# Kernel optimization log

Measured on AMD Instinct MI355X. Metric: run time of the kernel, lower is better.

## Reference

```python
import jax, jax.numpy as jnp
import numpy as np

N = 100_000        # nodes
E_HALF = 1_600_000 # undirected edges; symmetrized -> 3.2M directed
N_IN, N_HEMB, N_HGCN, N_OUT = 128, 32, 32, 1


def setup_inputs() -> dict:
    key = jax.random.key(0)
    ks = jax.random.split(key, 8)
    x = jax.random.normal(ks[0], (N, N_IN), dtype=jnp.float32)
    t = jax.random.uniform(ks[1], (N,), dtype=jnp.float32)
    # symmetric edge list (A = A^T), matching the typical undirected-graph usage
    src = jax.random.randint(ks[2], (E_HALF,), 0, N)
    dst = jax.random.randint(ks[3], (E_HALF,), 0, N)
    row = jnp.concatenate([src, dst]).astype(jnp.int32)
    col = jnp.concatenate([dst, src]).astype(jnp.int32)
    s = 0.05
    W_emb = jax.random.normal(ks[4], (N_IN, N_HEMB), jnp.float32) * s
    b_emb = jnp.zeros((N_HEMB,), jnp.float32)
    W_gcn = jax.random.normal(ks[5], (N_HEMB, N_HGCN), jnp.float32) * s
    b_gcn = jnp.zeros((N_HGCN,), jnp.float32)
    W1 = jax.random.normal(ks[6], (N_HGCN + 2, N_HEMB), jnp.float32) * s
    b1 = jnp.zeros((N_HEMB,), jnp.float32)
    W2 = jax.random.normal(ks[7], (N_HEMB, N_OUT), jnp.float32) * s
    b2 = jnp.zeros((N_OUT,), jnp.float32)
    return dict(x=x, t=t, row=row, col=col,
                W_emb=W_emb, b_emb=b_emb, W_gcn=W_gcn, b_gcn=b_gcn,
                W1=W1, b1=b1, W2=W2, b2=b2)


def reference(x, t, row, col, W_emb, b_emb, W_gcn, b_gcn, W1, b1, W2, b2):
    n = x.shape[0]
    h = jax.nn.relu(x @ W_emb + b_emb)                        # [N, Hemb]
    # per-edge attention score via gather + dot
    att = jnp.einsum('eh,eh->e', h[row], h[col])              # [E]
    att = jnp.exp(att - att.max())                            # global-max stabilized exp
    # per-node softmax denominator (segment sum over neighbors) + eps
    deno = jax.ops.segment_sum(att, row, num_segments=n) + 1e-8
    att = att / deno[row]                                     # normalized edge attention
    # exposure z: attention-weighted neighbor treatments
    z = jax.ops.segment_sum(att * t[col], row, num_segments=n)  # [N]
    # GCNConv (unit edge values: set_value() is non-inplace so adj_t stays valueless;
    # PyG then fills 1s, adds self loops, symmetric D^-1/2 norm)
    deg = jax.ops.segment_sum(jnp.ones(row.shape, jnp.float32), col, num_segments=n) + 1.0
    dis = jax.lax.rsqrt(deg)                                  # [N], deg >= 1
    hw = h @ W_gcn                                            # [N, Hgcn]
    msg = dis[row][:, None] * hw[row]                         # [E, Hgcn]
    agg = jax.ops.segment_sum(msg, col, num_segments=n)       # [N, Hgcn]
    gcn = dis[:, None] * agg + (dis * dis)[:, None] * hw + b_gcn
    rep = h + jax.nn.relu(gcn)                                # residual node rep
    feats = jnp.concatenate([rep, t[:, None], z[:, None]], axis=1)  # [N, Hgcn+2]
    out = jax.nn.relu(feats @ W1 + b1) @ W2 + b2              # [N, 1]
    return out, rep, z
```

## Files before the change

### kernel.cpp

```cpp
#include <hip/hip_runtime.h>
#include <hip/hip_bf16.h>

static constexpr int HN = 32;
static constexpr int NIN = 128;
static constexpr int CH1 = 8192;
static constexpr int CAP2 = 16384;

__device__ __forceinline__ float bf2f(unsigned short u) {
    union { unsigned int i; float f; } v;
    v.i = ((unsigned int)u) << 16;
    return v.f;
}
__device__ __forceinline__ float ldf(const void* p, size_t i, int isbf) {
    return isbf ? bf2f(((const unsigned short*)p)[i]) : ((const float*)p)[i];
}

__global__ void detect_kernel(const unsigned int* __restrict__ xw,
                              int* __restrict__ flag)
{
    int lane = threadIdx.x;
    int hits = 0;
    #pragma unroll
    for (int k = 0; k < 2; ++k) {
        unsigned int w = xw[lane + 64 * k];
        float a = bf2f((unsigned short)(w & 0xFFFFu));
        float aa = fabsf(a);
        if (a == 0.0f || (aa >= 0.000244140625f && aa <= 32.0f)) hits++;
    }
    #pragma unroll
    for (int m = 32; m; m >>= 1) hits += __shfl_xor(hits, m, 64);
    if (lane == 0) flag[0] = (hits >= 64) ? 1 : 0;
}

__global__ __launch_bounds__(256) void embed1_kernel(
    const void* __restrict__ x,
    const void* __restrict__ Wemb,
    const void* __restrict__ bemb,
    const int* __restrict__ flagp,
    float* __restrict__ h, int N)
{
    __shared__ float We[NIN * HN];
    __shared__ float be[HN];
    __shared__ float xs[32][NIN];
    const int tid = threadIdx.x;
    const int isbf = flagp[0];

    for (int i = tid; i < NIN * HN; i += 256) We[i] = ldf(Wemb, i, isbf);
    if (tid < HN) be[tid] = ldf(bemb, tid, isbf);

    const int n0 = blockIdx.x * 32;
    if (isbf) {
        const ushort4* x4 = (const ushort4*)((const unsigned short*)x + (size_t)n0 * NIN);
        for (int i = tid; i < 32 * (NIN / 4); i += 256) {
            ushort4 u = x4[i];
            int base = i * 4, n = base >> 7, k = base & (NIN - 1);
            xs[n][k] = bf2f(u.x); xs[n][k + 1] = bf2f(u.y);
            xs[n][k + 2] = bf2f(u.z); xs[n][k + 3] = bf2f(u.w);
        }
    } else {
        const float4* x4 = (const float4*)((const float*)x + (size_t)n0 * NIN);
        for (int i = tid; i < 32 * (NIN / 4); i += 256) {
            float4 u = x4[i];
            int base = i * 4, n = base >> 7, k = base & (NIN - 1);
            xs[n][k] = u.x; xs[n][k + 1] = u.y;
            xs[n][k + 2] = u.z; xs[n][k + 3] = u.w;
        }
    }
    __syncthreads();

    const int f = tid & 31, ns = tid >> 5;
    float a0 = be[f], a1 = be[f], a2 = be[f], a3 = be[f];
    #pragma unroll 8
    for (int k = 0; k < NIN; ++k) {
        float w = We[k * HN + f];
        a0 += xs[ns +  0][k] * w;
        a1 += xs[ns +  8][k] * w;
        a2 += xs[ns + 16][k] * w;
        a3 += xs[ns + 24][k] * w;
    }
    if (n0 + ns      < N) h[(size_t)(n0 + ns     ) * HN + f] = fmaxf(a0, 0.f);
    if (n0 + ns +  8 < N) h[(size_t)(n0 + ns +  8) * HN + f] = fmaxf(a1, 0.f);
    if (n0 + ns + 16 < N) h[(size_t)(n0 + ns + 16) * HN + f] = fmaxf(a2, 0.f);
    if (n0 + ns + 24 < N) h[(size_t)(n0 + ns + 24) * HN + f] = fmaxf(a3, 0.f);
}

__global__ __launch_bounds__(512) void bhist_kernel(
    const int* __restrict__ col, int* __restrict__ bucket_cnt, int E, int B)
{
    __shared__ int hist[512];
    const int t = threadIdx.x;
    const int e0 = blockIdx.x * CH1;
    for (int i = t; i < B; i += 512) hist[i] = 0;
    __syncthreads();
    #pragma unroll
    for (int k = 0; k < CH1 / 512; ++k) {
        int e = e0 + k * 512 + t;
        if (e < E) atomicAdd(&hist[col[e] >> 8], 1);
    }
    __syncthreads();
    for (int i = t; i < B; i += 512)
        if (hist[i]) atomicAdd(&bucket_cnt[i], hist[i]);
}

__global__ __launch_bounds__(512) void bscan_kernel(
    const int* __restrict__ bucket_cnt, int* __restrict__ bucket_base,
    int* __restrict__ bucket_cursor, int B, int E)
{
    __shared__ int sc[512];
    __shared__ int orig[512];
    const int t = threadIdx.x;
    int v0 = (t < B) ? bucket_cnt[t] : 0;
    sc[t] = v0; orig[t] = v0;
    __syncthreads();
    for (int o = 1; o < 512; o <<= 1) {
        int v = (t >= o) ? sc[t - o] : 0;
        __syncthreads();
        sc[t] += v;
        __syncthreads();
    }
    if (t < B) {
        int ex = sc[t] - orig[t];
        bucket_base[t] = ex;
        bucket_cursor[t] = ex;
    }
    if (t == 0) bucket_base[B] = E;
}

__global__ __launch_bounds__(512) void phase1_kernel(
    const int* __restrict__ row, const int* __restrict__ col,
    int* __restrict__ bucket_cursor, int* __restrict__ bucketed, int E, int B)
{
    __shared__ int hist[512];
    __shared__ int sc[512];
    __shared__ int cnt[512];
    __shared__ int gbase[512];
    __shared__ int word[CH1];
    __shared__ int dst[CH1];
    const int t = threadIdx.x;
    const int e0 = blockIdx.x * CH1;
    const int M = (E - e0 < CH1) ? (E - e0) : CH1;

    for (int i = t; i < B; i += 512) { hist[i] = 0; cnt[i] = 0; }
    __syncthreads();
    #pragma unroll
    for (int k = 0; k < CH1 / 512; ++k) {
        int e = e0 + k * 512 + t;
        if (e < E) atomicAdd(&hist[col[e] >> 8], 1);
    }
    __syncthreads();
    sc[t] = (t < B) ? hist[t] : 0;
    __syncthreads();
    for (int o = 1; o < 512; o <<= 1) {
        int v = (t >= o) ? sc[t - o] : 0;
        __syncthreads();
        sc[t] += v;
        __syncthreads();
    }
    if (t < B && hist[t])
        gbase[t] = atomicAdd(&bucket_cursor[t], hist[t]);
    __syncthreads();
    #pragma unroll
    for (int k = 0; k < CH1 / 512; ++k) {
        int e = e0 + k * 512 + t;
        if (e < E) {
            int c = col[e], r = row[e];
            int b = c >> 8;
            int lr = atomicAdd(&cnt[b], 1);
            int p = sc[b] - hist[b] + lr;
            word[p] = (r << 8) | (c & 255);
            dst[p] = gbase[b] + lr;
        }
    }
    __syncthreads();
    for (int i = t; i < M; i += 512)
        bucketed[dst[i]] = word[i];
}

__global__ __launch_bounds__(256) void phase2a_kernel(
    const int* __restrict__ bucketed, const int* __restrict__ bucket_base,
    int* __restrict__ count, int N)
{
    __shared__ int cnt[256];
    const int t = threadIdx.x, b = blockIdx.x;
    cnt[t] = 0;
    __syncthreads();
    const int s0 = bucket_base[b], s1 = bucket_base[b + 1];
    for (int i = s0 + t; i < s1; i += 256)
        atomicAdd(&cnt[bucketed[i] & 255], 1);
    __syncthreads();
    int node = (b << 8) + t;
    if (node < N) count[node] = cnt[t];
}

__global__ __launch_bounds__(256) void scan1_kernel(
    const int* __restrict__ count, int* __restrict__ bsum, int N)
{
    __shared__ int s[256];
    const int t = threadIdx.x, b = blockIdx.x;
    int base = b * 2048 + t * 8, sum = 0;
    #pragma unroll
    for (int k = 0; k < 8; ++k) { int i = base + k; if (i < N) sum += count[i]; }
    s[t] = sum; __syncthreads();
    for (int o = 128; o; o >>= 1) { if (t < o) s[t] += s[t + o]; __syncthreads(); }
    if (t == 0) bsum[b] = s[0];
}

__global__ void scan2_kernel(int* __restrict__ bsum, int nsb,
                             int* __restrict__ rowptr, int N, int E)
{
    if (threadIdx.x == 0 && blockIdx.x == 0) {
        int acc = 0;
        for (int i = 0; i < nsb; ++i) { int v = bsum[i]; bsum[i] = acc; acc += v; }
        rowptr[N] = E;
    }
}

__global__ __launch_bounds__(256) void scan3_kernel(
    int* __restrict__ countcur, const int* __restrict__ bsum,
    int* __restrict__ rowptr, int N)
{
    __shared__ int s[256];
    const int t = threadIdx.x, b = blockIdx.x;
    int base = b * 2048 + t * 8;
    int c[8]; int sum = 0;
    #pragma unroll
    for (int k = 0; k < 8; ++k) {
        int i = base + k;
        c[k] = (i < N) ? countcur[i] : 0;
        sum += c[k];
    }
    s[t] = sum; __syncthreads();
    for (int o = 1; o < 256; o <<= 1) {
        int v = (t >= o) ? s[t - o] : 0;
        __syncthreads();
        s[t] += v;
        __syncthreads();
    }
    int acc = bsum[b] + ((t == 0) ? 0 : s[t - 1]);
    #pragma unroll
    for (int k = 0; k < 8; ++k) {
        int i = base + k;
        if (i < N) { rowptr[i] = acc; countcur[i] = acc; acc += c[k]; }
    }
}

__global__ __launch_bounds__(256) void phase2b_kernel(
    const int* __restrict__ bucketed, const int* __restrict__ bucket_base,
    const int* __restrict__ rowptr, int* __restrict__ cursor,
    int* __restrict__ csr_src, int N)
{
    __shared__ int stage[CAP2];
    __shared__ int rps[257];
    __shared__ int cnt[256];
    const int t = threadIdx.x, b = blockIdx.x;
    const int s0 = bucket_base[b], s1 = bucket_base[b + 1];
    const int segsz = s1 - s0;
    const int node0 = b << 8;
    const int nodes = (N - node0 < 256) ? (N - node0) : 256;
    if (t <= nodes) rps[t] = rowptr[node0 + t];
    cnt[t] = 0;
    __syncthreads();
    if (segsz <= CAP2) {
        for (int i = s0 + t; i < s1; i += 256) {
            int w = bucketed[i];
            int lc = w & 255;
            int off = rps[lc] - s0 + atomicAdd(&cnt[lc], 1);
            stage[off] = w >> 8;
        }
        __syncthreads();
        for (int i = t; i < segsz; i += 256) csr_src[s0 + i] = stage[i];
    } else {
        for (int i = s0 + t; i < s1; i += 256) {
            int w = bucketed[i];
            int pos = atomicAdd(&cursor[node0 + (w & 255)], 1);
            csr_src[pos] = w >> 8;
        }
    }
}

__global__ __launch_bounds__(256) void embed2_kernel(
    const float* __restrict__ h, const void* __restrict__ Wgcn,
    const int* __restrict__ rowptr, const int* __restrict__ flagp,
    float* __restrict__ hws, int N)
{
    __shared__ float Wg[HN * HN];
    __shared__ float hs[32][HN + 1];
    const int tid = threadIdx.x;
    const int isbf = flagp[0];
    for (int i = tid; i < HN * HN; i += 256) Wg[i] = ldf(Wgcn, i, isbf);
    const int n0 = blockIdx.x * 32;
    for (int i = tid; i < 32 * HN; i += 256) {
        int n = i >> 5, f = i & 31;
        hs[n][f] = (n0 + n < N) ? h[(size_t)(n0 + n) * HN + f] : 0.f;
    }
    __syncthreads();
    const int f = tid & 31, ns = tid >> 5;
    #pragma unroll
    for (int g = 0; g < 4; ++g) {
        int n = ns + 8 * g, v = n0 + n;
        if (v < N) {
            float acc = 0.f;
            #pragma unroll
            for (int k = 0; k < HN; ++k) acc += hs[n][k] * Wg[k * HN + f];
            float dis = rsqrtf((float)(rowptr[v + 1] - rowptr[v]) + 1.0f);
            hws[(size_t)v * HN + f] = dis * acc;
        }
    }
}

__global__ __launch_bounds__(256) void passB_kernel(
    const float* __restrict__ h, const float* __restrict__ hws,
    const int* __restrict__ csr_src, const int* __restrict__ rowptr,
    const void* __restrict__ t, const void* __restrict__ bgcn,
    const int* __restrict__ flagp,
    float* __restrict__ outr, float* __restrict__ outz,
    float* __restrict__ out0_ml, float* __restrict__ denout, int N)
{
    const int tid = threadIdx.x;
    const int lane = tid & 31;
    const int sub = lane >> 3;
    const int j = lane & 7;
    const int v = blockIdx.x * 8 + (tid >> 5);
    if (v >= N) return;
    const int isbf = flagp[0];

    const float4* h4 = (const float4*)h;
    const float4* w4 = (const float4*)hws;
    float4 hv = h4[(size_t)v * 8 + j];
    float4 wsv = w4[(size_t)v * 8 + j];
    const int s = rowptr[v], e2 = rowptr[v + 1];

    float m = -1e30f, den = 0.f, num = 0.f;
    float ax = 0.f, ay = 0.f, az = 0.f, aw = 0.f;
    for (int i = s + sub; i < e2; i += 4) {
        int r = csr_src[i];
        float4 hr = h4[(size_t)r * 8 + j];
        float4 wr = w4[(size_t)r * 8 + j];
        float tr = ldf(t, r, isbf);
        float p = hv.x * hr.x + hv.y * hr.y + hv.z * hr.z + hv.w * hr.w;
        p += __shfl_xor(p, 1, 32);
        p += __shfl_xor(p, 2, 32);
        p += __shfl_xor(p, 4, 32);
        float mn = fmaxf(m, p);
        float corr = __expf(m - mn);
        float a = __expf(p - mn);
        den = den * corr + a;
        num = num * corr + a * tr;
        m = mn;
        ax += wr.x; ay += wr.y; az += wr.z; aw += wr.w;
    }
    #pragma unroll
    for (int o = 8; o <= 16; o <<= 1) {
        float mo = __shfl_xor(m, o, 32);
        float dno = __shfl_xor(den, o, 32);
        float nmo = __shfl_xor(num, o, 32);
        float mn = fmaxf(m, mo);
        float ca = __expf(m - mn), cb = __expf(mo - mn);
        den = den * ca + dno * cb;
        num = num * ca + nmo * cb;
        m = mn;
        ax += __shfl_xor(ax, o, 32);
        ay += __shfl_xor(ay, o, 32);
        az += __shfl_xor(az, o, 32);
        aw += __shfl_xor(aw, o, 32);
    }

    float dv = rsqrtf((float)(e2 - s) + 1.0f);
    float4 rep;
    rep.x = hv.x + fmaxf(dv * (ax + wsv.x) + ldf(bgcn, 4 * j + 0, isbf), 0.f);
    rep.y = hv.y + fmaxf(dv * (ay + wsv.y) + ldf(bgcn, 4 * j + 1, isbf), 0.f);
    rep.z = hv.z + fmaxf(dv * (az + wsv.z) + ldf(bgcn, 4 * j + 2, isbf), 0.f);
    rep.w = hv.w + fmaxf(dv * (aw + wsv.w) + ldf(bgcn, 4 * j + 3, isbf), 0.f);
    if (sub == 0)
        ((float4*)outr)[(size_t)v * 8 + j] = rep;
    if (lane == 0) {
        outz[v]    = num / fmaxf(den, 1e-37f);
        out0_ml[v] = m;
        denout[v]  = den;
    }
}

__global__ __launch_bounds__(256) void amax1_kernel(
    const float* __restrict__ ml, float* __restrict__ bmax2, int N)
{
    float m = -INFINITY;
    for (int i = blockIdx.x * 256 + threadIdx.x; i < N; i += 256 * 256)
        m = fmaxf(m, ml[i]);
    #pragma unroll
    for (int s = 32; s; s >>= 1) m = fmaxf(m, __shfl_xor(m, s, 64));
    __shared__ float sm[4];
    if ((threadIdx.x & 63) == 0) sm[threadIdx.x >> 6] = m;
    __syncthreads();
    if (threadIdx.x == 0)
        bmax2[blockIdx.x] = fmaxf(fmaxf(sm[0], sm[1]), fmaxf(sm[2], sm[3]));
}
__global__ __launch_bounds__(256) void amax2_kernel(
    const float* __restrict__ bmax2, float* __restrict__ amax)
{
    float m = bmax2[threadIdx.x];
    #pragma unroll
    for (int s = 32; s; s >>= 1) m = fmaxf(m, __shfl_xor(m, s, 64));
    __shared__ float sm[4];
    if ((threadIdx.x & 63) == 0) sm[threadIdx.x >> 6] = m;
    __syncthreads();
    if (threadIdx.x == 0) amax[0] = fmaxf(fmaxf(sm[0], sm[1]), fmaxf(sm[2], sm[3]));
}

__global__ __launch_bounds__(256) void final_kernel(
    const float* __restrict__ rep_in,
    const void* __restrict__ t, const int* __restrict__ flagp,
    const float* __restrict__ amax, const float* __restrict__ denarr,
    const void* __restrict__ W1, const void* __restrict__ b1,
    const void* __restrict__ W2, const void* __restrict__ b2,
    float* __restrict__ out0, float* __restrict__ outz, int N)
{
    __shared__ float W1s[34 * HN];
    __shared__ float b1s[HN], W2s[HN];
    __shared__ float b2s;
    const int tid = threadIdx.x;
    const int isbf = flagp[0];
    for (int i = tid; i < 34 * HN; i += 256) W1s[i] = ldf(W1, i, isbf);
    if (tid < HN) {
        b1s[tid] = ldf(b1, tid, isbf);
        W2s[tid] = ldf(W2, tid, isbf);
    }
    if (tid == 0) b2s = ldf(b2, 0, isbf);
    __syncthreads();

    const int lane = tid & 31;
    const int v = blockIdx.x * 8 + (tid >> 5);
    if (v >= N) return;

    float rep = rep_in[(size_t)v * HN + lane];
    float ml  = out0[v];
    float den = denarr[v];
    float zh  = outz[v];
    float am  = amax[0];
    float term = (1e-8f / den) * expf(am - ml);
    float z = zh / (1.0f + term);
    float tv = ldf(t, v, isbf);

    float acc = b1s[lane] + tv * W1s[32 * HN + lane] + z * W1s[33 * HN + lane];
    #pragma unroll
    for (int k = 0; k < HN; ++k)
        acc += __shfl(rep, k, 32) * W1s[k * HN + lane];
    float f1 = fmaxf(acc, 0.f);
    float o = f1 * W2s[lane];
    #pragma unroll
    for (int m = 16; m; m >>= 1) o += __shfl_xor(o, m, 32);

    if (lane == 0) {
        out0[v] = o + b2s;
        outz[v] = z;
    }
}

extern "C" void kernel_launch(void* const* d_in, const int* in_sizes, int n_in,
                              void* d_out, int out_size, void* d_ws, size_t ws_size,
                              hipStream_t stream)
{
    const int N = out_size / 34;
    const int E = in_sizes[2];

    const void* x    = d_in[0];
    const void* t    = d_in[1];
    const int* row   = (const int*)d_in[2];
    const int* col   = (const int*)d_in[3];
    const void* Wemb = d_in[4];
    const void* bemb = d_in[5];
    const void* Wgcn = d_in[6];
    const void* bgcn = d_in[7];
    const void* W1   = d_in[8];
    const void* b1   = d_in[9];
    const void* W2   = d_in[10];
    const void* b2   = d_in[11];

    const int B   = (N + 255) >> 8;
    const int nsb = (N + 2047) / 2048;
    const int NB1 = (E + CH1 - 1) / CH1;

    char* wsb = (char*)d_ws;
    size_t off = 0;
    float* h        = (float*)(wsb + off); off += (size_t)N * HN * 4;
    size_t hwbytes  = (size_t)N * HN * 4;
    if ((size_t)E * 4 > hwbytes) hwbytes = (size_t)E * 4;
    char*  hwreg    = wsb + off;           off += hwbytes;
    int*   csr_src  = (int*)(wsb + off);   off += (size_t)E * 4;
    int*   rowptr   = (int*)(wsb + off);   off += (size_t)(N + 1) * 4;
    int*   count    = (int*)(wsb + off);   off += (size_t)N * 4;
    int*   bucket_cnt    = (int*)(wsb + off); off += (size_t)B * 4;
    int*   bucket_base   = (int*)(wsb + off); off += (size_t)(B + 1) * 4;
    int*   bucket_cursor = (int*)(wsb + off); off += (size_t)B * 4;
    float* bmax2    = (float*)(wsb + off); off += 256 * 4;
    int*   bsum     = (int*)(wsb + off);   off += (size_t)nsb * 4;
    float* amax     = (float*)(wsb + off); off += 4;
    int*   flag     = (int*)(wsb + off);   off += 4;

    int*   bucketed = (int*)hwreg;
    float* hws      = (float*)hwreg;

    hipMemsetAsync(bucket_cnt, 0, (size_t)B * 4, stream);

    detect_kernel<<<1, 64, 0, stream>>>((const unsigned int*)x, flag);
    embed1_kernel<<<(N + 31) / 32, 256, 0, stream>>>(x, Wemb, bemb, flag, h, N);

    bhist_kernel<<<NB1, 512, 0, stream>>>(col, bucket_cnt, E, B);
    bscan_kernel<<<1, 512, 0, stream>>>(bucket_cnt, bucket_base,
                                        bucket_cursor, B, E);
    phase1_kernel<<<NB1, 512, 0, stream>>>(row, col, bucket_cursor,
                                           bucketed, E, B);
    phase2a_kernel<<<B, 256, 0, stream>>>(bucketed, bucket_base, count, N);
    scan1_kernel<<<nsb, 256, 0, stream>>>(count, bsum, N);
    scan2_kernel<<<1, 64, 0, stream>>>(bsum, nsb, rowptr, N, E);
    scan3_kernel<<<nsb, 256, 0, stream>>>(count, bsum, rowptr, N);
    phase2b_kernel<<<B, 256, 0, stream>>>(bucketed, bucket_base, rowptr,
                                          count, csr_src, N);
    embed2_kernel<<<(N + 31) / 32, 256, 0, stream>>>(h, Wgcn, rowptr, flag,
                                                     hws, N);

    float* outp = (float*)d_out;
    float* out0 = outp;
    float* outr = outp + N;
    float* outz = outp + (size_t)N * 33;
    float* den  = (float*)count;

    passB_kernel<<<(N + 7) / 8, 256, 0, stream>>>(
        h, hws, csr_src, rowptr, t, bgcn, flag, outr, outz, out0, den, N);
    amax1_kernel<<<256, 256, 0, stream>>>(out0, bmax2, N);
    amax2_kernel<<<1, 256, 0, stream>>>(bmax2, amax);
    final_kernel<<<(N + 7) / 8, 256, 0, stream>>>(
        outr, t, flag, amax, den, W1, b1, W2, b2, out0, outz, N);
}
```

Before: 402.3 us.

## Fuse CSR build into single per-bucket kernel and simplify bucket scatter

The per-bucket count, the three global scan kernels and the staged CSR scatter are merged into one phase2 kernel. It computes node row offsets locally from bucket_base plus an in-block scan and scatters directly to csr_src. Phase1 drops its LDS staging and local prefix scan and writes bucketed words straight to global memory using per-bucket atomic slots. passB gains a one-step software prefetch of the next neighbor index. This cuts several kernel launches and LDS pressure, at the cost of less coalesced global writes in phase1 and phase2.

```diff
diff --git a/kernel.cpp b/kernel.cpp
--- a/kernel.cpp
+++ b/kernel.cpp
@@ -4,7 +4,6 @@
 static constexpr int HN = 32;
 static constexpr int NIN = 128;
 static constexpr int CH1 = 8192;
-static constexpr int CAP2 = 16384;
 
 __device__ __forceinline__ float bf2f(unsigned short u) {
     union { unsigned int i; float f; } v;
@@ -131,16 +130,11 @@
     int* __restrict__ bucket_cursor, int* __restrict__ bucketed, int E, int B)
 {
     __shared__ int hist[512];
-    __shared__ int sc[512];
-    __shared__ int cnt[512];
     __shared__ int gbase[512];
-    __shared__ int word[CH1];
-    __shared__ int dst[CH1];
     const int t = threadIdx.x;
     const int e0 = blockIdx.x * CH1;
-    const int M = (E - e0 < CH1) ? (E - e0) : CH1;
-
-    for (int i = t; i < B; i += 512) { hist[i] = 0; cnt[i] = 0; }
+
+    for (int i = t; i < B; i += 512) hist[i] = 0;
     __syncthreads();
     #pragma unroll
     for (int k = 0; k < CH1 / 512; ++k) {
@@ -148,16 +142,11 @@
         if (e < E) atomicAdd(&hist[col[e] >> 8], 1);
     }
     __syncthreads();
-    sc[t] = (t < B) ? hist[t] : 0;
-    __syncthreads();
-    for (int o = 1; o < 512; o <<= 1) {
-        int v = (t >= o) ? sc[t - o] : 0;
-        __syncthreads();
-        sc[t] += v;
-        __syncthreads();
-    }
-    if (t < B && hist[t])
-        gbase[t] = atomicAdd(&bucket_cursor[t], hist[t]);
+    for (int i = t; i < B; i += 512) {
+        int hc = hist[i];
+        gbase[i] = hc ? atomicAdd(&bucket_cursor[i], hc) : 0;
+        hist[i] = 0;
+    }
     __syncthreads();
     #pragma unroll
     for (int k = 0; k < CH1 / 512; ++k) {
@@ -165,116 +154,48 @@
         if (e < E) {
             int c = col[e], r = row[e];
             int b = c >> 8;
-            int lr = atomicAdd(&cnt[b], 1);
-            int p = sc[b] - hist[b] + lr;
-            word[p] = (r << 8) | (c & 255);
-            dst[p] = gbase[b] + lr;
+            int lr = atomicAdd(&hist[b], 1);
+            bucketed[gbase[b] + lr] = (r << 8) | (c & 255);
         }
     }
-    __syncthreads();
-    for (int i = t; i < M; i += 512)
-        bucketed[dst[i]] = word[i];
-}
-
-__global__ __launch_bounds__(256) void phase2a_kernel(
+}
+
+__global__ __launch_bounds__(256) void phase2_kernel(
     const int* __restrict__ bucketed, const int* __restrict__ bucket_base,
-    int* __restrict__ count, int N)
+    int* __restrict__ rowptr, int* __restrict__ csr_src, int N, int E)
 {
     __shared__ int cnt[256];
+    __shared__ int sc[256];
+    __shared__ int base[256];
     const int t = threadIdx.x, b = blockIdx.x;
+    const int s0 = bucket_base[b], s1 = bucket_base[b + 1];
+    const int node0 = b << 8;
     cnt[t] = 0;
     __syncthreads();
-    const int s0 = bucket_base[b], s1 = bucket_base[b + 1];
     for (int i = s0 + t; i < s1; i += 256)
         atomicAdd(&cnt[bucketed[i] & 255], 1);
     __syncthreads();
-    int node = (b << 8) + t;
-    if (node < N) count[node] = cnt[t];
-}
-
-__global__ __launch_bounds__(256) void scan1_kernel(
-    const int* __restrict__ count, int* __restrict__ bsum, int N)
-{
-    __shared__ int s[256];
-    const int t = threadIdx.x, b = blockIdx.x;
-    int base = b * 2048 + t * 8, sum = 0;
-    #pragma unroll
-    for (int k = 0; k < 8; ++k) { int i = base + k; if (i < N) sum += count[i]; }
-    s[t] = sum; __syncthreads();
-    for (int o = 128; o; o >>= 1) { if (t < o) s[t] += s[t + o]; __syncthreads(); }
-    if (t == 0) bsum[b] = s[0];
-}
-
-__global__ void scan2_kernel(int* __restrict__ bsum, int nsb,
-                             int* __restrict__ rowptr, int N, int E)
-{
-    if (threadIdx.x == 0 && blockIdx.x == 0) {
-        int acc = 0;
-        for (int i = 0; i < nsb; ++i) { int v = bsum[i]; bsum[i] = acc; acc += v; }
-        rowptr[N] = E;
-    }
-}
-
-__global__ __launch_bounds__(256) void scan3_kernel(
-    int* __restrict__ countcur, const int* __restrict__ bsum,
-    int* __restrict__ rowptr, int N)
-{
-    __shared__ int s[256];
-    const int t = threadIdx.x, b = blockIdx.x;
-    int base = b * 2048 + t * 8;
-    int c[8]; int sum = 0;
-    #pragma unroll
-    for (int k = 0; k < 8; ++k) {
-        int i = base + k;
-        c[k] = (i < N) ? countcur[i] : 0;
-        sum += c[k];
-    }
-    s[t] = sum; __syncthreads();
+    int myc = cnt[t];
+    sc[t] = myc;
+    __syncthreads();
     for (int o = 1; o < 256; o <<= 1) {
-        int v = (t >= o) ? s[t - o] : 0;
+        int v = (t >= o) ? sc[t - o] : 0;
         __syncthreads();
-        s[t] += v;
+        sc[t] += v;
         __syncthreads();
     }
-    int acc = bsum[b] + ((t == 0) ? 0 : s[t - 1]);
-    #pragma unroll
-    for (int k = 0; k < 8; ++k) {
-        int i = base + k;
-        if (i < N) { rowptr[i] = acc; countcur[i] = acc; acc += c[k]; }
-    }
-}
-
-__global__ __launch_bounds__(256) void phase2b_kernel(
-    const int* __restrict__ bucketed, const int* __restrict__ bucket_base,
-    const int* __restrict__ rowptr, int* __restrict__ cursor,
-    int* __restrict__ csr_src, int N)
-{
-    __shared__ int stage[CAP2];
-    __shared__ int rps[257];
-    __shared__ int cnt[256];
-    const int t = threadIdx.x, b = blockIdx.x;
-    const int s0 = bucket_base[b], s1 = bucket_base[b + 1];
-    const int segsz = s1 - s0;
-    const int node0 = b << 8;
-    const int nodes = (N - node0 < 256) ? (N - node0) : 256;
-    if (t <= nodes) rps[t] = rowptr[node0 + t];
+    int ex = s0 + sc[t] - myc;
+    base[t] = ex;
+    int node = node0 + t;
+    if (node < N) rowptr[node] = ex;
+    if (b == (int)gridDim.x - 1 && t == 0) rowptr[N] = E;
     cnt[t] = 0;
     __syncthreads();
-    if (segsz <= CAP2) {
-        for (int i = s0 + t; i < s1; i += 256) {
-            int w = bucketed[i];
-            int lc = w & 255;
-            int off = rps[lc] - s0 + atomicAdd(&cnt[lc], 1);
-            stage[off] = w >> 8;
-        }
-        __syncthreads();
-        for (int i = t; i < segsz; i += 256) csr_src[s0 + i] = stage[i];
-    } else {
-        for (int i = s0 + t; i < s1; i += 256) {
-            int w = bucketed[i];
-            int pos = atomicAdd(&cursor[node0 + (w & 255)], 1);
-            csr_src[pos] = w >> 8;
-        }
+    for (int i = s0 + t; i < s1; i += 256) {
+        int w = bucketed[i];
+        int lc = w & 255;
+        int pos = base[lc] + atomicAdd(&cnt[lc], 1);
+        csr_src[pos] = w >> 8;
     }
 }
 
@@ -332,8 +253,11 @@
 
     float m = -1e30f, den = 0.f, num = 0.f;
     float ax = 0.f, ay = 0.f, az = 0.f, aw = 0.f;
-    for (int i = s + sub; i < e2; i += 4) {
-        int r = csr_src[i];
+    int i = s + sub;
+    int r = (i < e2) ? csr_src[i] : 0;
+    while (i < e2) {
+        int in = i + 4;
+        int rn = (in < e2) ? csr_src[in] : 0;
         float4 hr = h4[(size_t)r * 8 + j];
         float4 wr = w4[(size_t)r * 8 + j];
         float tr = ldf(t, r, isbf);
@@ -348,6 +272,7 @@
         num = num * corr + a * tr;
         m = mn;
         ax += wr.x; ay += wr.y; az += wr.z; aw += wr.w;
+        i = in; r = rn;
     }
     #pragma unroll
     for (int o = 8; o <= 16; o <<= 1) {
@@ -476,7 +401,6 @@
     const void* b2   = d_in[11];
 
     const int B   = (N + 255) >> 8;
-    const int nsb = (N + 2047) / 2048;
     const int NB1 = (E + CH1 - 1) / CH1;
 
     char* wsb = (char*)d_ws;
@@ -487,12 +411,11 @@
     char*  hwreg    = wsb + off;           off += hwbytes;
     int*   csr_src  = (int*)(wsb + off);   off += (size_t)E * 4;
     int*   rowptr   = (int*)(wsb + off);   off += (size_t)(N + 1) * 4;
-    int*   count    = (int*)(wsb + off);   off += (size_t)N * 4;
+    float* den      = (float*)(wsb + off); off += (size_t)N * 4;
     int*   bucket_cnt    = (int*)(wsb + off); off += (size_t)B * 4;
     int*   bucket_base   = (int*)(wsb + off); off += (size_t)(B + 1) * 4;
     int*   bucket_cursor = (int*)(wsb + off); off += (size_t)B * 4;
     float* bmax2    = (float*)(wsb + off); off += 256 * 4;
-    int*   bsum     = (int*)(wsb + off);   off += (size_t)nsb * 4;
     float* amax     = (float*)(wsb + off); off += 4;
     int*   flag     = (int*)(wsb + off);   off += 4;
 
@@ -509,12 +432,8 @@
                                         bucket_cursor, B, E);
     phase1_kernel<<<NB1, 512, 0, stream>>>(row, col, bucket_cursor,
                                            bucketed, E, B);
-    phase2a_kernel<<<B, 256, 0, stream>>>(bucketed, bucket_base, count, N);
-    scan1_kernel<<<nsb, 256, 0, stream>>>(count, bsum, N);
-    scan2_kernel<<<1, 64, 0, stream>>>(bsum, nsb, rowptr, N, E);
-    scan3_kernel<<<nsb, 256, 0, stream>>>(count, bsum, rowptr, N);
-    phase2b_kernel<<<B, 256, 0, stream>>>(bucketed, bucket_base, rowptr,
-                                          count, csr_src, N);
+    phase2_kernel<<<B, 256, 0, stream>>>(bucketed, bucket_base, rowptr,
+                                         csr_src, N, E);
     embed2_kernel<<<(N + 31) / 32, 256, 0, stream>>>(h, Wgcn, rowptr, flag,
                                                      hws, N);
 
@@ -522,7 +441,6 @@
     float* out0 = outp;
     float* outr = outp + N;
     float* outz = outp + (size_t)N * 33;
-    float* den  = (float*)count;
 
     passB_kernel<<<(N + 7) / 8, 256, 0, stream>>>(
         h, hws, csr_src, rowptr, t, bgcn, flag, outr, outz, out0, den, N);
```

Result: slower. 419.2 us (+4.2%).
